# Performance work log

Hardware: AMD Instinct MI355X
Metric: run time of the kernel (lower is better)

## Reference

```python
import jax, jax.numpy as jnp
import numpy as np

N = 50000      # nodes
E = 800000     # edges
D_IN = 128
D_OUT = 128
R = 8          # relation types
EPS = 1e-12    # F.normalize eps


def setup_inputs() -> dict:
    key = jax.random.key(0)
    ks = jax.random.split(key, 10)
    s_in = 1.0 / np.sqrt(D_IN)
    s_out = 1.0 / np.sqrt(D_OUT)
    return {
        "x": jax.random.normal(ks[0], (N, D_IN), jnp.float32),
        "W1": jax.random.normal(ks[1], (R, D_IN, D_OUT), jnp.float32) * s_in,
        "loopW1": jax.random.normal(ks[2], (D_IN, D_OUT), jnp.float32) * s_in,
        "b1": jax.random.normal(ks[3], (D_OUT,), jnp.float32) * 0.01,
        "W2": jax.random.normal(ks[4], (R, D_OUT, D_OUT), jnp.float32) * s_out,
        "loopW2": jax.random.normal(ks[5], (D_OUT, D_OUT), jnp.float32) * s_out,
        "b2": jax.random.normal(ks[6], (D_OUT,), jnp.float32) * 0.01,
        "src": jax.random.randint(ks[7], (E,), 0, N),
        "dst": jax.random.randint(ks[8], (E,), 0, N),
        "etypes": jax.random.randint(ks[9], (E,), 0, R),
    }


def rel_layer(x, src, dst, etypes, W, loopW, b):
    # transform every node by every relation: [R, N, D_out]
    xw = jnp.einsum('ni,rio->rno', x, W)
    # gather per-edge messages: [E, D_out]
    msg = xw[etypes, src]
    # scatter-add to destination nodes
    agg = jax.ops.segment_sum(msg, dst, num_segments=x.shape[0])
    # self-loop + bias (DGL RelGraphConv defaults)
    return agg + x @ loopW + b


def reference(x, W1, loopW1, b1, W2, loopW2, b2, src, dst, etypes):
    h = jax.nn.relu(rel_layer(x, src, dst, etypes, W1, loopW1, b1))
    h = rel_layer(h, src, dst, etypes, W2, loopW2, b2)
    # F.normalize: row-wise L2, eps=1e-12
    nrm = jnp.maximum(jnp.linalg.norm(h, axis=1, keepdims=True), EPS)
    return h / nrm
```

## Files before the change

kernel.cpp:

```cpp
#include <hip/hip_runtime.h>
#include <hip/hip_bf16.h>

#define D 128
#define CH 4096
#define BM 16

typedef unsigned int u32;
typedef unsigned short u16;
typedef __attribute__((ext_vector_type(8))) short s16x8;
typedef __attribute__((ext_vector_type(4))) float f32x4;
typedef __attribute__((ext_vector_type(2))) float f32x2;

__device__ __forceinline__ float bf2f(u16 u) {
    union { u32 u; float f; } v; v.u = ((u32)u) << 16; return v.f;
}
__device__ __forceinline__ u16 f2bf(float f) {
    union { float f; u32 u; } v; v.f = f;
    return (u16)((v.u + 0x7fffu + ((v.u >> 16) & 1u)) >> 16);
}
__device__ __forceinline__ u32 pack_bf2(float a, float b) {
    __hip_bfloat162 t = __float22bfloat162_rn(make_float2(a, b));
    union { __hip_bfloat162 t; u32 u; } v; v.t = t; return v.u;
}
__device__ __forceinline__ void unpack2(u32 u, float& lo, float& hi) {
    union { u32 u; float f; } a, b;
    a.u = u << 16; b.u = u & 0xffff0000u;
    lo = a.f; hi = b.f;
}

__global__ void detect_dtype(const u16* __restrict__ x, int* __restrict__ flag,
                             int* __restrict__ gcnt, int nbuck) {
    __shared__ int cnt;
    if (threadIdx.x == 0) cnt = 0;
    __syncthreads();
    if ((int)threadIdx.x < nbuck) gcnt[threadIdx.x] = 0;
    u16 u = x[2 * threadIdx.x];
    int e = (u >> 7) & 0xFF;
    if (e >= 96 && e <= 150) atomicAdd(&cnt, 1);
    __syncthreads();
    if (threadIdx.x == 0) *flag = (cnt >= 128) ? 0 : 1;
}

__global__ __launch_bounds__(256)
void to_bf16_all(const void* __restrict__ s0, const void* __restrict__ s1,
                 const void* __restrict__ s2, const void* __restrict__ s3,
                 const void* __restrict__ s4, const void* __restrict__ s5,
                 const void* __restrict__ s6,
                 u16* __restrict__ d0, u16* __restrict__ d1, u16* __restrict__ d2,
                 u16* __restrict__ d3, u16* __restrict__ d4, u16* __restrict__ d5,
                 u16* __restrict__ d6,
                 long long n0, long long n1, long long n2, long long n3,
                 long long n4, long long n5, long long n6,
                 const int* __restrict__ flag)
{
    if (*flag == 0) return;
    long long i = (long long)blockIdx.x * 256 + threadIdx.x;
    const void* s; u16* d; long long off;
    if      (i < n0)                   { s = s0; d = d0; off = i; }
    else if (i < n0+n1)                { s = s1; d = d1; off = i-n0; }
    else if (i < n0+n1+n2)             { s = s2; d = d2; off = i-n0-n1; }
    else if (i < n0+n1+n2+n3)          { s = s3; d = d3; off = i-n0-n1-n2; }
    else if (i < n0+n1+n2+n3+n4)       { s = s4; d = d4; off = i-n0-n1-n2-n3; }
    else if (i < n0+n1+n2+n3+n4+n5)    { s = s5; d = d5; off = i-n0-n1-n2-n3-n4; }
    else if (i < n0+n1+n2+n3+n4+n5+n6) { s = s6; d = d6; off = i-n0-n1-n2-n3-n4-n5; }
    else return;
    d[off] = f2bf(((const float*)s)[off]);
}

__global__ __launch_bounds__(256)
void csr_count(const int* __restrict__ dst, int* __restrict__ gcnt, int E, int nbuck) {
    __shared__ int scnt[256];
    int tid = threadIdx.x;
    scnt[tid] = 0;
    __syncthreads();
    int base = blockIdx.x * CH;
#pragma unroll
    for (int it = 0; it < CH / 256; ++it) {
        int e = base + it * 256 + tid;
        if (e < E) atomicAdd(&scnt[dst[e] >> 8], 1);
    }
    __syncthreads();
    if (tid < nbuck && scnt[tid] > 0) atomicAdd(&gcnt[tid], scnt[tid]);
}

__global__ __launch_bounds__(256)
void csr_scan(const int* __restrict__ gcnt, int* __restrict__ bstart, int* __restrict__ bcur,
              int nbuck, int N_, int E_, int* __restrict__ offs) {
    __shared__ int wpart[4];
    int tid = threadIdx.x, lane = tid & 63, wid = tid >> 6;
    int v = (tid < nbuck) ? gcnt[tid] : 0;
    int s = v;
#pragma unroll
    for (int off = 1; off < 64; off <<= 1) {
        int t = __shfl_up(s, off, 64);
        if (lane >= off) s += t;
    }
    if (lane == 63) wpart[wid] = s;
    __syncthreads();
    int add = 0;
    for (int w = 0; w < wid; ++w) add += wpart[w];
    int excl = add + s - v;
    if (tid <= nbuck) bstart[tid] = excl;
    if (tid < nbuck)  bcur[tid]  = excl;
    if (tid == 0) offs[N_] = E_;
}

__global__ __launch_bounds__(256)
void csr_part(const int* __restrict__ src, const int* __restrict__ dst,
              const int* __restrict__ et, int* __restrict__ bcur,
              u32* __restrict__ ebuf, int E, int N, int nbuck) {
    __shared__ int scnt[256], sbase[256];
    int tid = threadIdx.x;
    scnt[tid] = 0;
    __syncthreads();
    int base = blockIdx.x * CH;
#pragma unroll
    for (int it = 0; it < CH / 256; ++it) {
        int e = base + it * 256 + tid;
        if (e < E) atomicAdd(&scnt[dst[e] >> 8], 1);
    }
    __syncthreads();
    if (tid < nbuck) {
        int c = scnt[tid];
        sbase[tid] = c ? atomicAdd(&bcur[tid], c) : 0;
    }
    __syncthreads();
    scnt[tid] = 0;
    __syncthreads();
#pragma unroll
    for (int it = 0; it < CH / 256; ++it) {
        int e = base + it * 256 + tid;
        if (e >= E) continue;
        int d = dst[e];
        int b = d >> 8;
        int p = sbase[b] + atomicAdd(&scnt[b], 1);
        ebuf[p] = ((u32)(d & 255) << 24) | ((u32)et[e] << 16) | (u32)src[e];
    }
}

__global__ __launch_bounds__(256)
void csr_emit(const u32* __restrict__ ebuf, const int* __restrict__ bstart,
              int* __restrict__ offs, int* __restrict__ rowidx, int N) {
    __shared__ int hist[2048], excl[2048], cur[2048];
    __shared__ int wpart[4];
    int b = blockIdx.x, tid = threadIdx.x;
    int lo = bstart[b], hi = bstart[b + 1];
    for (int i = tid; i < 2048; i += 256) { hist[i] = 0; cur[i] = 0; }
    __syncthreads();
    for (int i = lo + tid; i < hi; i += 256) {
        u32 rec = ebuf[i];
        int key = (int)((rec >> 24) << 3) | (int)((rec >> 16) & 7u);
        atomicAdd(&hist[key], 1);
    }
    __syncthreads();
    int loc[8]; int tsum = 0;
#pragma unroll
    for (int k = 0; k < 8; ++k) { loc[k] = tsum; tsum += hist[tid * 8 + k]; }
    int lane = tid & 63, wid = tid >> 6;
    int s = tsum;
#pragma unroll
    for (int off = 1; off < 64; off <<= 1) {
        int t = __shfl_up(s, off, 64);
        if (lane >= off) s += t;
    }
    if (lane == 63) wpart[wid] = s;
    __syncthreads();
    int add = 0;
    for (int w = 0; w < wid; ++w) add += wpart[w];
    int tex = add + s - tsum;
#pragma unroll
    for (int k = 0; k < 8; ++k) excl[tid * 8 + k] = tex + loc[k];
    int node = (b << 8) + tid;
    if (node < N) offs[node] = lo + tex;
    __syncthreads();
    for (int i = lo + tid; i < hi; i += 256) {
        u32 rec = ebuf[i];
        int key = (int)((rec >> 24) << 3) | (int)((rec >> 16) & 7u);
        int p = lo + excl[key] + atomicAdd(&cur[key], 1);
        rowidx[p] = (int)(rec & 0xFFFFFFu);
    }
}

__global__ __launch_bounds__(256)
void build_wt(const u16* __restrict__ W1c, const u16* __restrict__ W1o,
              const u16* __restrict__ lW1c, const u16* __restrict__ lW1o,
              const u16* __restrict__ W2c, const u16* __restrict__ W2o,
              const u16* __restrict__ lW2c, const u16* __restrict__ lW2o,
              const int* __restrict__ flag, int R_, u16* __restrict__ wt)
{
    __shared__ u32 st[8192];
    bool f = (*flag != 0);
    int m = blockIdx.x;
    int layer = m / 9, c = m % 9;
    const u16* src;
    if (layer == 0) src = (c < R_) ? ((f ? W1c : W1o) + (size_t)c * D * D) : (f ? lW1c : lW1o);
    else            src = (c < R_) ? ((f ? W2c : W2o) + (size_t)c * D * D) : (f ? lW2c : lW2o);
    int tid = threadIdx.x;
    const u32* s32 = (const u32*)src;
    for (int i = tid; i < 8192; i += 256) st[i] = s32[i];
    __syncthreads();
    const u16* st16 = (const u16*)st;
    u16* dstp = wt + (size_t)m * 16384;
    for (int i = tid; i < 16384; i += 256) {
        int wvv = i >> 11;
        int ks  = (i >> 9) & 3;
        int ln  = (i >> 3) & 63;
        int j   = i & 7;
        int k   = ks * 32 + (ln >> 4) * 8 + j;
        int col = wvv * 16 + (ln & 15);
        dstp[i] = st16[k * 128 + col];
    }
}

__device__ __forceinline__ void gather_row(const u32* __restrict__ X32,
                                           const int* __restrict__ rowidx,
                                           u32* __restrict__ plane,
                                           int j0, int j1, int rl, int lane, int vrec)
{
    int deg = j1 - j0;
    if (deg <= 0) return;
    const int vsw = (((lane >> 2) ^ rl) << 2) | (lane & 3);
    int ecur = -1;
    float a0 = 0.f, a1 = 0.f;
    int base = j0;
    for (;;) {
        int wend = j1 - base; if (wend > 64) wend = 64;
        int pos = 0;
        while (pos < wend) {
            int nb = wend - pos; if (nb > 16) nb = 16;
            int srec[16]; u32 g[16];
#pragma unroll
            for (int k = 0; k < 16; ++k)
                if (k < nb) srec[k] = __builtin_amdgcn_readlane(vrec, pos + k);
#pragma unroll
            for (int k = 0; k < 16; ++k)
                if (k < nb) g[k] = X32[(size_t)(srec[k] & 0xffff) * 64 + lane];
#pragma unroll
            for (int k = 0; k < 16; ++k) {
                if (k < nb) {
                    int et = srec[k] >> 16;
                    if (et != ecur) {
                        if (ecur >= 0) plane[(ecur * BM + rl) * 64 + vsw] = pack_bf2(a0, a1);
                        ecur = et; a0 = 0.f; a1 = 0.f;
                    }
                    float lo_, hi_;
                    unpack2(g[k], lo_, hi_);
                    a0 += lo_; a1 += hi_;
                }
            }
            pos += nb;
        }
        base += wend;
        if (base >= j1) break;
        vrec = rowidx[(base + lane < j1) ? base + lane : j1 - 1];
    }
    plane[(ecur * BM + rl) * 64 + vsw] = pack_bf2(a0, a1);
}

__global__ __launch_bounds__(512, 8)
void rel_layer_fused(const u16* __restrict__ xc, const u16* __restrict__ xo,
                     const int* __restrict__ offs, const int* __restrict__ rowidx,
                     const u16* __restrict__ wt,
                     const u16* __restrict__ bc, const u16* __restrict__ bo,
                     const int* __restrict__ flag,
                     int M, int R_, int mode, void* __restrict__ out)
{
    __shared__ u16 As[9 * BM * D];
    const bool f = (*flag != 0);
    const u16* X    = f ? xc : xo;
    const u16* bias = f ? bc : bo;

    const int row0 = blockIdx.x * BM;
    const int tid  = threadIdx.x;
    const int lane = tid & 63;
    const int wv   = tid >> 6;
    const int quad = lane >> 4;
    const int l16  = lane & 15;

    if (wv < 4) {
        auto* lds0 = (__attribute__((address_space(3))) char*)As;
        int rl = wv * 4 + quad;
        int rg = row0 + rl; if (rg >= M) rg = M - 1;
        int cg = l16 ^ rl;
        const u16* gp = X + (size_t)rg * D + cg * 8;
        __builtin_amdgcn_global_load_lds(
            (const __attribute__((address_space(1))) void*)gp,
            (__attribute__((address_space(3))) void*)(lds0 + 8 * BM * 256 + wv * 1024),
            16, 0, 0);
    }

    {
        u32* pz = (u32*)As;
        int rbase = wv * 2;
#pragma unroll
        for (int pl = 0; pl < 8; ++pl)
#pragma unroll
            for (int rr = 0; rr < 2; ++rr)
                pz[(pl * BM + rbase + rr) * 64 + lane] = 0;
    }

    {
        const u32* X32 = (const u32*)X;
        u32* plane = (u32*)As;
        int rlA = wv * 2, rlB = rlA + 1;
        int rA = row0 + rlA, rB = row0 + rlB;
        int iA0 = rA < M ? rA : M, iA1 = rA + 1 < M ? rA + 1 : M;
        int iB0 = rB < M ? rB : M, iB1 = rB + 1 < M ? rB + 1 : M;
        int jA0 = offs[iA0], jA1 = offs[iA1];
        int jB0 = offs[iB0], jB1 = offs[iB1];
        int vrecA = 0, vrecB = 0;
        if (jA1 > jA0) vrecA = rowidx[(jA0 + lane < jA1) ? jA0 + lane : jA1 - 1];
        if (jB1 > jB0) vrecB = rowidx[(jB0 + lane < jB1) ? jB0 + lane : jB1 - 1];
        gather_row(X32, rowidx, plane, jA0, jA1, rlA, lane, vrecA);
        gather_row(X32, rowidx, plane, jB0, jB1, rlB, lane, vrecB);
    }

    __syncthreads();

    f32x4 acc = (f32x4)0.f;
    for (int c = 0; c <= R_; ++c) {
        int cidx = (c < R_) ? c : 8;
        const u16* Bt = wt + (size_t)cidx * 16384 + (size_t)wv * 2048 + lane * 8;
        s16x8 bfr[4];
#pragma unroll
        for (int ks = 0; ks < 4; ++ks)
            bfr[ks] = *(const s16x8*)(Bt + ks * 512);
#pragma unroll
        for (int ks = 0; ks < 4; ++ks) {
            int chp = (ks * 4 + quad) ^ l16;
            s16x8 a = *(const s16x8*)(As + (cidx * BM + l16) * D + chp * 8);
            acc = __builtin_amdgcn_mfma_f32_16x16x32_bf16(a, bfr[ks], acc, 0, 0, 0);
        }
    }

    const int col = wv * 16 + l16;
    const float b = bf2f(bias[col]);

    if (mode == 0) {
        u32* o = (u32*)out;
#pragma unroll
        for (int i = 0; i < 4; ++i) {
            int r = row0 + quad * 4 + i;
            float v = fmaxf(acc[i] + b, 0.f);
            float vp = __shfl_xor(v, 1, 64);
            if (!(l16 & 1) && r < M)
                o[(size_t)r * 64 + (col >> 1)] = pack_bf2(v, vp);
        }
    } else {
        float v[4];
        float pr[4];
#pragma unroll
        for (int i = 0; i < 4; ++i) {
            v[i] = acc[i] + b;
            float p = v[i] * v[i];
            p += __shfl_xor(p, 1, 64);
            p += __shfl_xor(p, 2, 64);
            p += __shfl_xor(p, 4, 64);
            p += __shfl_xor(p, 8, 64);
            pr[i] = p;
        }
        __syncthreads();
        float* fs = (float*)As;
        if (l16 == 0) {
#pragma unroll
            for (int i = 0; i < 4; ++i) fs[(quad * 4 + i) * 8 + wv] = pr[i];
        }
        __syncthreads();
        if (tid < 16) {
            float s = 0.f;
#pragma unroll
            for (int w = 0; w < 8; ++w) s += fs[tid * 8 + w];
            fs[128 + tid] = 1.f / fmaxf(sqrtf(s), 1e-12f);
        }
        __syncthreads();
#pragma unroll
        for (int i = 0; i < 4; ++i) {
            int rl = quad * 4 + i;
            int r = row0 + rl;
            float sc = fs[128 + rl];
            float a0 = v[i] * sc;
            float ap = __shfl_xor(a0, 1, 64);
            if (!(l16 & 1) && r < M) {
                if (f) {
                    f32x2 w; w[0] = a0; w[1] = ap;
                    ((f32x2*)out)[(size_t)r * 64 + (col >> 1)] = w;
                } else {
                    ((u32*)out)[(size_t)r * 64 + (col >> 1)] = pack_bf2(a0, ap);
                }
            }
        }
    }
}

static inline size_t align256(size_t x) { return (x + 255) & ~(size_t)255; }

extern "C" void kernel_launch(void* const* d_in, const int* in_sizes, int n_in,
                              void* d_out, int out_size, void* d_ws, size_t ws_size,
                              hipStream_t stream)
{
    const void* x_in   = d_in[0];
    const void* W1_in  = d_in[1];
    const void* lW1_in = d_in[2];
    const void* b1_in  = d_in[3];
    const void* W2_in  = d_in[4];
    const void* lW2_in = d_in[5];
    const void* b2_in  = d_in[6];
    const int* src = (const int*)d_in[7];
    const int* dst = (const int*)d_in[8];
    const int* et  = (const int*)d_in[9];

    const int N = in_sizes[0] / D;
    const int E = in_sizes[7];
    const int R = in_sizes[1] / (D * D);
    const int nbuck = (N + 255) >> 8;

    const long long ND  = (long long)N * D;
    const long long RDD = (long long)R * D * D;
    const long long DDl = (long long)D * D;

    size_t off = 0;
    auto alloc = [&](size_t bytes) { size_t o = off; off = align256(off + bytes); return o; };
    size_t o_flag = alloc(256);
    size_t o_xc   = alloc((size_t)ND * 2);
    size_t o_W1   = alloc((size_t)RDD * 2);
    size_t o_lW1  = alloc((size_t)DDl * 2);
    size_t o_b1   = alloc((size_t)D * 2);
    size_t o_W2   = alloc((size_t)RDD * 2);
    size_t o_lW2  = alloc((size_t)DDl * 2);
    size_t o_b2   = alloc((size_t)D * 2);
    size_t o_h    = alloc((size_t)ND * 2);
    size_t o_offs = alloc((size_t)(N + 1) * 4);
    size_t o_gcnt = alloc(1024);
    size_t o_bst  = alloc(1040 * 4);
    size_t o_bcur = alloc(1024);
    size_t o_ebuf = alloc((size_t)E * 4);
    size_t o_ridx = alloc((size_t)E * 4);
    size_t o_wt   = alloc((size_t)2 * 9 * D * D * 2);
    (void)ws_size;

    char* ws = (char*)d_ws;
    int* flag   = (int*)(ws + o_flag);
    u16* x_c    = (u16*)(ws + o_xc);
    u16* W1c    = (u16*)(ws + o_W1);
    u16* lW1c   = (u16*)(ws + o_lW1);
    u16* b1c    = (u16*)(ws + o_b1);
    u16* W2c    = (u16*)(ws + o_W2);
    u16* lW2c   = (u16*)(ws + o_lW2);
    u16* b2c    = (u16*)(ws + o_b2);
    u16* h      = (u16*)(ws + o_h);
    int* offs   = (int*)(ws + o_offs);
    int* gcnt   = (int*)(ws + o_gcnt);
    int* bstart = (int*)(ws + o_bst);
    int* bcur   = (int*)(ws + o_bcur);
    u32* ebuf   = (u32*)(ws + o_ebuf);
    int* rowidx = (int*)(ws + o_ridx);
    u16* wt     = (u16*)(ws + o_wt);

    dim3 blk(256, 1, 1);
    int mb    = (N + BM - 1) / BM;
    int nblkE = (E + CH - 1) / CH;
    auto cdiv = [](long long n) { return (u32)((n + 255) / 256); };

    detect_dtype<<<dim3(1), blk, 0, stream>>>((const u16*)x_in, flag, gcnt, nbuck);
    long long tot = ND + RDD + DDl + D + RDD + DDl + D;
    to_bf16_all<<<dim3(cdiv(tot)), blk, 0, stream>>>(
        x_in, W1_in, lW1_in, b1_in, W2_in, lW2_in, b2_in,
        x_c, W1c, lW1c, b1c, W2c, lW2c, b2c,
        ND, RDD, DDl, (long long)D, RDD, DDl, (long long)D, flag);

    build_wt<<<dim3(18), blk, 0, stream>>>(
        W1c, (const u16*)W1_in, lW1c, (const u16*)lW1_in,
        W2c, (const u16*)W2_in, lW2c, (const u16*)lW2_in, flag, R, wt);

    csr_count<<<dim3(nblkE), blk, 0, stream>>>(dst, gcnt, E, nbuck);
    csr_scan<<<dim3(1), blk, 0, stream>>>(gcnt, bstart, bcur, nbuck, N, E, offs);
    csr_part<<<dim3(nblkE), blk, 0, stream>>>(src, dst, et, bcur, ebuf, E, N, nbuck);
    csr_emit<<<dim3(nbuck), blk, 0, stream>>>(ebuf, bstart, offs, rowidx, N);

    rel_layer_fused<<<dim3(mb), dim3(512), 0, stream>>>(
        x_c, (const u16*)x_in, offs, rowidx, wt,
        b1c, (const u16*)b1_in, flag, N, R, 0, h);

    rel_layer_fused<<<dim3(mb), dim3(512), 0, stream>>>(
        h, h, offs, rowidx, wt + (size_t)9 * D * D,
        b2c, (const u16*)b2_in, flag, N, R, 1, d_out);
}
```

Measured before the change: 304.7 us.

## Vectorize x conversion, convert weights inside build_wt, merge two-row gather loop

The all-inputs fp32-to-bf16 conversion kernel is replaced by a float4-vectorized conversion of x only. build_wt now reads and converts the raw weights itself, and bias is read directly in its raw dtype, which removes the intermediate bf16 weight buffers and the extra pass over them. The per-row gather is also merged so each wave walks the contiguous edge range of its two rows in one loop. To make that work, rowidx records now carry a combined (row, etype) key in the upper bits and only 19 bits of source index. That limits supported node counts and drops the shared-memory staging in build_wt, which now reads weights uncoalesced.

```diff
diff --git a/kernel.cpp b/kernel.cpp
--- a/kernel.cpp
+++ b/kernel.cpp
@@ -10,6 +10,7 @@
 typedef __attribute__((ext_vector_type(8))) short s16x8;
 typedef __attribute__((ext_vector_type(4))) float f32x4;
 typedef __attribute__((ext_vector_type(2))) float f32x2;
+typedef __attribute__((ext_vector_type(2))) u32 u32x2;
 
 __device__ __forceinline__ float bf2f(u16 u) {
     union { u32 u; float f; } v; v.u = ((u32)u) << 16; return v.f;
@@ -42,29 +43,17 @@
 }
 
 __global__ __launch_bounds__(256)
-void to_bf16_all(const void* __restrict__ s0, const void* __restrict__ s1,
-                 const void* __restrict__ s2, const void* __restrict__ s3,
-                 const void* __restrict__ s4, const void* __restrict__ s5,
-                 const void* __restrict__ s6,
-                 u16* __restrict__ d0, u16* __restrict__ d1, u16* __restrict__ d2,
-                 u16* __restrict__ d3, u16* __restrict__ d4, u16* __restrict__ d5,
-                 u16* __restrict__ d6,
-                 long long n0, long long n1, long long n2, long long n3,
-                 long long n4, long long n5, long long n6,
-                 const int* __restrict__ flag)
+void to_bf16_x(const float4* __restrict__ xin, u32x2* __restrict__ xout,
+               long long n4, const int* __restrict__ flag)
 {
     if (*flag == 0) return;
     long long i = (long long)blockIdx.x * 256 + threadIdx.x;
-    const void* s; u16* d; long long off;
-    if      (i < n0)                   { s = s0; d = d0; off = i; }
-    else if (i < n0+n1)                { s = s1; d = d1; off = i-n0; }
-    else if (i < n0+n1+n2)             { s = s2; d = d2; off = i-n0-n1; }
-    else if (i < n0+n1+n2+n3)          { s = s3; d = d3; off = i-n0-n1-n2; }
-    else if (i < n0+n1+n2+n3+n4)       { s = s4; d = d4; off = i-n0-n1-n2-n3; }
-    else if (i < n0+n1+n2+n3+n4+n5)    { s = s5; d = d5; off = i-n0-n1-n2-n3-n4; }
-    else if (i < n0+n1+n2+n3+n4+n5+n6) { s = s6; d = d6; off = i-n0-n1-n2-n3-n4-n5; }
-    else return;
-    d[off] = f2bf(((const float*)s)[off]);
+    if (i >= n4) return;
+    float4 v = xin[i];
+    u32x2 o;
+    o[0] = pack_bf2(v.x, v.y);
+    o[1] = pack_bf2(v.z, v.w);
+    xout[i] = o;
 }
 
 __global__ __launch_bounds__(256)
@@ -177,29 +166,23 @@
         u32 rec = ebuf[i];
         int key = (int)((rec >> 24) << 3) | (int)((rec >> 16) & 7u);
         int p = lo + excl[key] + atomicAdd(&cur[key], 1);
-        rowidx[p] = (int)(rec & 0xFFFFFFu);
-    }
-}
-
-__global__ __launch_bounds__(256)
-void build_wt(const u16* __restrict__ W1c, const u16* __restrict__ W1o,
-              const u16* __restrict__ lW1c, const u16* __restrict__ lW1o,
-              const u16* __restrict__ W2c, const u16* __restrict__ W2o,
-              const u16* __restrict__ lW2c, const u16* __restrict__ lW2o,
+        rowidx[p] = (int)(((rec >> 24) & 31u) << 19) | (int)(rec & 0x7FFFFu);
+    }
+}
+
+__global__ __launch_bounds__(256)
+void build_wt(const void* __restrict__ W1r, const void* __restrict__ lW1r,
+              const void* __restrict__ W2r, const void* __restrict__ lW2r,
               const int* __restrict__ flag, int R_, u16* __restrict__ wt)
 {
-    __shared__ u32 st[8192];
     bool f = (*flag != 0);
     int m = blockIdx.x;
     int layer = m / 9, c = m % 9;
-    const u16* src;
-    if (layer == 0) src = (c < R_) ? ((f ? W1c : W1o) + (size_t)c * D * D) : (f ? lW1c : lW1o);
-    else            src = (c < R_) ? ((f ? W2c : W2o) + (size_t)c * D * D) : (f ? lW2c : lW2o);
+    size_t esz = f ? 4 : 2;
+    const char* src;
+    if (layer == 0) src = (c < R_) ? ((const char*)W1r + (size_t)c * D * D * esz) : (const char*)lW1r;
+    else            src = (c < R_) ? ((const char*)W2r + (size_t)c * D * D * esz) : (const char*)lW2r;
     int tid = threadIdx.x;
-    const u32* s32 = (const u32*)src;
-    for (int i = tid; i < 8192; i += 256) st[i] = s32[i];
-    __syncthreads();
-    const u16* st16 = (const u16*)st;
     u16* dstp = wt + (size_t)m * 16384;
     for (int i = tid; i < 16384; i += 256) {
         int wvv = i >> 11;
@@ -208,67 +191,22 @@
         int j   = i & 7;
         int k   = ks * 32 + (ln >> 4) * 8 + j;
         int col = wvv * 16 + (ln & 15);
-        dstp[i] = st16[k * 128 + col];
-    }
-}
-
-__device__ __forceinline__ void gather_row(const u32* __restrict__ X32,
-                                           const int* __restrict__ rowidx,
-                                           u32* __restrict__ plane,
-                                           int j0, int j1, int rl, int lane, int vrec)
-{
-    int deg = j1 - j0;
-    if (deg <= 0) return;
-    const int vsw = (((lane >> 2) ^ rl) << 2) | (lane & 3);
-    int ecur = -1;
-    float a0 = 0.f, a1 = 0.f;
-    int base = j0;
-    for (;;) {
-        int wend = j1 - base; if (wend > 64) wend = 64;
-        int pos = 0;
-        while (pos < wend) {
-            int nb = wend - pos; if (nb > 16) nb = 16;
-            int srec[16]; u32 g[16];
-#pragma unroll
-            for (int k = 0; k < 16; ++k)
-                if (k < nb) srec[k] = __builtin_amdgcn_readlane(vrec, pos + k);
-#pragma unroll
-            for (int k = 0; k < 16; ++k)
-                if (k < nb) g[k] = X32[(size_t)(srec[k] & 0xffff) * 64 + lane];
-#pragma unroll
-            for (int k = 0; k < 16; ++k) {
-                if (k < nb) {
-                    int et = srec[k] >> 16;
-                    if (et != ecur) {
-                        if (ecur >= 0) plane[(ecur * BM + rl) * 64 + vsw] = pack_bf2(a0, a1);
-                        ecur = et; a0 = 0.f; a1 = 0.f;
-                    }
-                    float lo_, hi_;
-                    unpack2(g[k], lo_, hi_);
-                    a0 += lo_; a1 += hi_;
-                }
-            }
-            pos += nb;
-        }
-        base += wend;
-        if (base >= j1) break;
-        vrec = rowidx[(base + lane < j1) ? base + lane : j1 - 1];
-    }
-    plane[(ecur * BM + rl) * 64 + vsw] = pack_bf2(a0, a1);
+        int idx = k * 128 + col;
+        dstp[i] = f ? f2bf(((const float*)src)[idx]) : ((const u16*)src)[idx];
+    }
 }
 
 __global__ __launch_bounds__(512, 8)
 void rel_layer_fused(const u16* __restrict__ xc, const u16* __restrict__ xo,
                      const int* __restrict__ offs, const int* __restrict__ rowidx,
                      const u16* __restrict__ wt,
-                     const u16* __restrict__ bc, const u16* __restrict__ bo,
+                     const void* __restrict__ bias_raw,
                      const int* __restrict__ flag,
                      int M, int R_, int mode, void* __restrict__ out)
 {
     __shared__ u16 As[9 * BM * D];
     const bool f = (*flag != 0);
-    const u16* X    = f ? xc : xo;
-    const u16* bias = f ? bc : bo;
+    const u16* X = f ? xc : xo;
 
     const int row0 = blockIdx.x * BM;
     const int tid  = threadIdx.x;
@@ -302,17 +240,50 @@
     {
         const u32* X32 = (const u32*)X;
         u32* plane = (u32*)As;
-        int rlA = wv * 2, rlB = rlA + 1;
-        int rA = row0 + rlA, rB = row0 + rlB;
-        int iA0 = rA < M ? rA : M, iA1 = rA + 1 < M ? rA + 1 : M;
-        int iB0 = rB < M ? rB : M, iB1 = rB + 1 < M ? rB + 1 : M;
-        int jA0 = offs[iA0], jA1 = offs[iA1];
-        int jB0 = offs[iB0], jB1 = offs[iB1];
-        int vrecA = 0, vrecB = 0;
-        if (jA1 > jA0) vrecA = rowidx[(jA0 + lane < jA1) ? jA0 + lane : jA1 - 1];
-        if (jB1 > jB0) vrecB = rowidx[(jB0 + lane < jB1) ? jB0 + lane : jB1 - 1];
-        gather_row(X32, rowidx, plane, jA0, jA1, rlA, lane, vrecA);
-        gather_row(X32, rowidx, plane, jB0, jB1, rlB, lane, vrecB);
+        int rA = row0 + wv * 2;
+        int i0 = rA < M ? rA : M;
+        int i1 = rA + 2 < M ? rA + 2 : M;
+        int j0 = offs[i0], j1 = offs[i1];
+        int key = -1;
+        float a0 = 0.f, a1 = 0.f;
+        int base = j0;
+        while (base < j1) {
+            int wlen = j1 - base; if (wlen > 64) wlen = 64;
+            int vrec = rowidx[base + (lane < wlen ? lane : wlen - 1)];
+            for (int pos = 0; pos < wlen; pos += 16) {
+                int nb = wlen - pos; if (nb > 16) nb = 16;
+                int sr[16]; u32 g[16];
+#pragma unroll
+                for (int k = 0; k < 16; ++k)
+                    if (k < nb) sr[k] = __builtin_amdgcn_readlane(vrec, pos + k);
+#pragma unroll
+                for (int k = 0; k < 16; ++k)
+                    if (k < nb) g[k] = (X32 + ((u32)(sr[k] & 0xffff) << 6))[lane];
+#pragma unroll
+                for (int k = 0; k < 16; ++k) {
+                    if (k < nb) {
+                        int nk = sr[k] >> 16;
+                        if (nk != key) {
+                            if (key >= 0) {
+                                int rl = ((key >> 3) - row0) & 31;
+                                int vsw = (((lane >> 2) ^ rl) << 2) | (lane & 3);
+                                plane[((key & 7) * BM + rl) * 64 + vsw] = pack_bf2(a0, a1);
+                            }
+                            key = nk; a0 = 0.f; a1 = 0.f;
+                        }
+                        float lo_, hi_;
+                        unpack2(g[k], lo_, hi_);
+                        a0 += lo_; a1 += hi_;
+                    }
+                }
+            }
+            base += wlen;
+        }
+        if (key >= 0) {
+            int rl = ((key >> 3) - row0) & 31;
+            int vsw = (((lane >> 2) ^ rl) << 2) | (lane & 3);
+            plane[((key & 7) * BM + rl) * 64 + vsw] = pack_bf2(a0, a1);
+        }
     }
 
     __syncthreads();
@@ -334,7 +305,8 @@
     }
 
     const int col = wv * 16 + l16;
-    const float b = bf2f(bias[col]);
+    const float b = f ? ((const float*)bias_raw)[col]
+                      : bf2f(((const u16*)bias_raw)[col]);
 
     if (mode == 0) {
         u32* o = (u32*)out;
@@ -414,20 +386,12 @@
     const int R = in_sizes[1] / (D * D);
     const int nbuck = (N + 255) >> 8;
 
-    const long long ND  = (long long)N * D;
-    const long long RDD = (long long)R * D * D;
-    const long long DDl = (long long)D * D;
+    const long long ND = (long long)N * D;
 
     size_t off = 0;
     auto alloc = [&](size_t bytes) { size_t o = off; off = align256(off + bytes); return o; };
     size_t o_flag = alloc(256);
     size_t o_xc   = alloc((size_t)ND * 2);
-    size_t o_W1   = alloc((size_t)RDD * 2);
-    size_t o_lW1  = alloc((size_t)DDl * 2);
-    size_t o_b1   = alloc((size_t)D * 2);
-    size_t o_W2   = alloc((size_t)RDD * 2);
-    size_t o_lW2  = alloc((size_t)DDl * 2);
-    size_t o_b2   = alloc((size_t)D * 2);
     size_t o_h    = alloc((size_t)ND * 2);
     size_t o_offs = alloc((size_t)(N + 1) * 4);
     size_t o_gcnt = alloc(1024);
@@ -441,12 +405,6 @@
     char* ws = (char*)d_ws;
     int* flag   = (int*)(ws + o_flag);
     u16* x_c    = (u16*)(ws + o_xc);
-    u16* W1c    = (u16*)(ws + o_W1);
-    u16* lW1c   = (u16*)(ws + o_lW1);
-    u16* b1c    = (u16*)(ws + o_b1);
-    u16* W2c    = (u16*)(ws + o_W2);
-    u16* lW2c   = (u16*)(ws + o_lW2);
-    u16* b2c    = (u16*)(ws + o_b2);
     u16* h      = (u16*)(ws + o_h);
     int* offs   = (int*)(ws + o_offs);
     int* gcnt   = (int*)(ws + o_gcnt);
@@ -459,18 +417,15 @@
     dim3 blk(256, 1, 1);
     int mb    = (N + BM - 1) / BM;
     int nblkE = (E + CH - 1) / CH;
-    auto cdiv = [](long long n) { return (u32)((n + 255) / 256); };
 
     detect_dtype<<<dim3(1), blk, 0, stream>>>((const u16*)x_in, flag, gcnt, nbuck);
-    long long tot = ND + RDD + DDl + D + RDD + DDl + D;
-    to_bf16_all<<<dim3(cdiv(tot)), blk, 0, stream>>>(
-        x_in, W1_in, lW1_in, b1_in, W2_in, lW2_in, b2_in,
-        x_c, W1c, lW1c, b1c, W2c, lW2c, b2c,
-        ND, RDD, DDl, (long long)D, RDD, DDl, (long long)D, flag);
+
+    long long n4 = ND / 4;
+    to_bf16_x<<<dim3((u32)((n4 + 255) / 256)), blk, 0, stream>>>(
+        (const float4*)x_in, (u32x2*)x_c, n4, flag);
 
     build_wt<<<dim3(18), blk, 0, stream>>>(
-        W1c, (const u16*)W1_in, lW1c, (const u16*)lW1_in,
-        W2c, (const u16*)W2_in, lW2c, (const u16*)lW2_in, flag, R, wt);
+        W1_in, lW1_in, W2_in, lW2_in, flag, R, wt);
 
     csr_count<<<dim3(nblkE), blk, 0, stream>>>(dst, gcnt, E, nbuck);
     csr_scan<<<dim3(1), blk, 0, stream>>>(gcnt, bstart, bcur, nbuck, N, E, offs);
@@ -479,9 +434,9 @@
 
     rel_layer_fused<<<dim3(mb), dim3(512), 0, stream>>>(
         x_c, (const u16*)x_in, offs, rowidx, wt,
-        b1c, (const u16*)b1_in, flag, N, R, 0, h);
+        b1_in, flag, N, R, 0, h);
 
     rel_layer_fused<<<dim3(mb), dim3(512), 0, stream>>>(
         h, h, offs, rowidx, wt + (size_t)9 * D * D,
-        b2c, (const u16*)b2_in, flag, N, R, 1, d_out);
-}
+        b2_in, flag, N, R, 1, d_out);
+}
```

New measurement: 284.8 us. 6.5% less time.
